# Kernel optimization log

Hardware: AMD Instinct MI355X
Metric: run time of the kernel (lower is better)

The kernel has to match this reference:

```python
import jax, jax.numpy as jnp
import numpy as np

B, L, H = 64, 512, 512  # batch_size, input_size (src len), hidden_size


def setup_inputs() -> dict:
    key = jax.random.key(0)
    ks = jax.random.split(key, 12)
    return {
        "encoder_outputs": jax.random.normal(ks[0], (B, L, H), dtype=jnp.float32),
        "attn_mask": jax.random.randint(ks[1], (B, L), 0, 2, dtype=jnp.int64),
        "hidden": jax.random.normal(ks[2], (B, H), dtype=jnp.float32),
        "coverage": jax.random.uniform(ks[3], (B, L), dtype=jnp.float32),
        # attnLin: Linear(H, H)
        "attn_w": jax.random.normal(ks[4], (H, H), dtype=jnp.float32) * 0.02,
        "attn_b": jax.random.normal(ks[5], (H,), dtype=jnp.float32) * 0.02,
        # decoderAttnLinear: Linear(H, H)
        "dec_w": jax.random.normal(ks[6], (H, H), dtype=jnp.float32) * 0.02,
        "dec_b": jax.random.normal(ks[7], (H,), dtype=jnp.float32) * 0.02,
        # cvgConv: Conv2d(L, L, kernel=(1, H), padding='same') -> weight [L, L, 1, H]
        "cvg_w": jax.random.normal(ks[8], (L, L, 1, H), dtype=jnp.float32) * 0.02,
        "cvg_b": jax.random.normal(ks[9], (L,), dtype=jnp.float32) * 0.02,
        # v parameter (trunc_normal in torch; plain normal is fine as a baseline)
        "v": jax.random.normal(ks[10], (B, H), dtype=jnp.float32),
    }


def reference(encoder_outputs, attn_mask, hidden, coverage,
              attn_w, attn_b, dec_w, dec_b, cvg_w, cvg_b, v):
    # Per-position linear loop in torch == one batched linear over [B, L, H].
    enc_feat = jnp.einsum('blh,oh->blo', encoder_outputs, attn_w) + attn_b  # [B,L,H]
    dec_feat = (hidden @ dec_w.T + dec_b)[:, None, :]                        # [B,1,H]
    # Coverage conv: input is [B, L(channels), 1, 1]; kernel (1, H) with 'same'
    # padding means only kernel column kw = (H-1)//2 ever overlaps the single
    # real (non-zero-padded) pixel, so the conv reduces exactly to a matmul
    # with that weight column plus bias. Same math, no wasted zero-multiplies.
    center = (H - 1) // 2
    w_eff = cvg_w[:, :, 0, center]                                           # [L_out, L_in]
    cov_feat = (coverage @ w_eff.T + cvg_b)[:, :, None]                      # [B,L,1]
    feats = jnp.tanh(enc_feat + dec_feat + cov_feat)                         # [B,L,H]
    scores = jnp.einsum('blh,bh->bl', feats, v)                              # [B,L]
    scores = jnp.where(attn_mask == 1, scores, -jnp.inf)
    attn_weights = jax.nn.softmax(scores, axis=1)                            # [B,L]
    new_coverage = coverage + attn_weights                                   # coverage += aw
    context_vector = jnp.einsum('bl,blh->bh', attn_weights, encoder_outputs) # [B,H]
    return context_vector, attn_weights, new_coverage
```

## Files before the change

### kernel.cpp

```cpp
#include <hip/hip_runtime.h>

#define B_ 64
#define L_ 512
#define H_ 512
#define CENTER 255

typedef float  f32x4  __attribute__((ext_vector_type(4)));
typedef _Float16 f16x8 __attribute__((ext_vector_type(8)));
typedef unsigned short u16x4 __attribute__((ext_vector_type(4)));
typedef unsigned short USH;


__device__ __forceinline__ float fast_tanh(float x) {
    float e = __expf(2.0f * x);
    return 1.0f - 2.0f * __builtin_amdgcn_rcpf(e + 1.0f);
}

__launch_bounds__(512)
__global__ void pre_kernel(const float* __restrict__ cvg_w, const float* __restrict__ cvg_b,
                           const float* __restrict__ coverage,
                           const float* __restrict__ aw, USH* __restrict__ bh16,
                           const float* __restrict__ hidden, const float* __restrict__ dec_w,
                           const float* __restrict__ dec_b,
                           float* __restrict__ dec_feat, float* __restrict__ cov_feat) {
    __shared__ float pool[34304];
    const int bid = blockIdx.x, t = threadIdx.x;
    if (bid < 512) {
        float* wl = pool;
        float* cs = pool + 512;
        const int i = bid;
        wl[t] = cvg_w[((size_t)(i * L_ + t)) * H_ + CENTER];
        #pragma unroll 8
        for (int c = 0; c < 64; ++c)
            cs[t * 65 + c] = coverage[c * L_ + t];
        __syncthreads();
        const int b = t >> 3, jg = t & 7;
        float sum = 0.f;
        #pragma unroll 8
        for (int jj = 0; jj < 64; ++jj) {
            int j = jg * 64 + ((jj + jg * 8) & 63);
            sum += cs[j * 65 + b] * wl[j];
        }
        sum += __shfl_xor(sum, 1, 64);
        sum += __shfl_xor(sum, 2, 64);
        sum += __shfl_xor(sum, 4, 64);
        if (jg == 0) cov_feat[b * L_ + i] = sum + cvg_b[i];
    } else if (bid < 640) {
        int i = (bid - 512) * 512 + t;
        float4 x = *(const float4*)&aw[(size_t)i * 4];
        float xs[4] = {x.x, x.y, x.z, x.w};
        u16x4 h;
        #pragma unroll
        for (int j = 0; j < 4; ++j)
            h[j] = __builtin_bit_cast(USH, (_Float16)xs[j]);
        *(u16x4*)&bh16[(size_t)i * 4] = h;
    } else {
        float* sbuf = pool;
        float* pr   = pool + 512;
        const int blk = bid - 640, b = blk >> 2, qq = blk & 3;
        const int ol = t & 127, part = t >> 7;
        sbuf[t] = hidden[b * H_ + t];
        __syncthreads();
        const float* row  = dec_w + (size_t)(qq * 128 + ol) * H_ + part * 128;
        const float* hseg = sbuf + part * 128;
        float d0 = 0.f, d1 = 0.f, d2 = 0.f, d3 = 0.f;
        #pragma unroll
        for (int k = 0; k < 128; k += 16) {
            float4 w0 = *(const float4*)&row[k];
            float4 w1 = *(const float4*)&row[k + 4];
            float4 w2 = *(const float4*)&row[k + 8];
            float4 w3 = *(const float4*)&row[k + 12];
            d0 += w0.x * hseg[k]      + w0.y * hseg[k + 1]  + w0.z * hseg[k + 2]  + w0.w * hseg[k + 3];
            d1 += w1.x * hseg[k + 4]  + w1.y * hseg[k + 5]  + w1.z * hseg[k + 6]  + w1.w * hseg[k + 7];
            d2 += w2.x * hseg[k + 8]  + w2.y * hseg[k + 9]  + w2.z * hseg[k + 10] + w2.w * hseg[k + 11];
            d3 += w3.x * hseg[k + 12] + w3.y * hseg[k + 13] + w3.z * hseg[k + 14] + w3.w * hseg[k + 15];
        }
        pr[t] = d0 + d1 + d2 + d3;
        __syncthreads();
        if (t < 128)
            dec_feat[b * H_ + qq * 128 + t] = pr[t] + pr[t + 128] + pr[t + 256] + pr[t + 384]
                                              + dec_b[qq * 128 + t];
    }
}

#define BM 128

#define STAGE_B(BUF, KS1)                                                                  \
    {                                                                                      \
        _Pragma("unroll")                                                                  \
        for (int it = 0; it < 2; ++it)                                                     \
            __builtin_amdgcn_global_load_lds(                                              \
                (const __attribute__((address_space(1))) void*)(bh16 + goffB[it] + (KS1) * 32), \
                (__attribute__((address_space(3))) void*)&Bsh[BUF][(wv * 2 + it) * 512],   \
                16, 0, 0);                                                                 \
    }

#define CVTWRITEA(BUF, A4)                                                                 \
    {                                                                                      \
        float axs[4] = {A4.x, A4.y, A4.z, A4.w};                                           \
        u16x4 hh;                                                                          \
        _Pragma("unroll")                                                                  \
        for (int j = 0; j < 4; ++j)                                                        \
            hh[j] = __builtin_bit_cast(USH, (_Float16)axs[j]);                             \
        *(u16x4*)&Ash[BUF][awoff] = hh;                                                    \
    }

__launch_bounds__(1024, 4)
__global__ void fused_score_mfma(const float* __restrict__ enc,
                                 const USH* __restrict__ bh16,
                                 const float* __restrict__ attn_b,
                                 const float* __restrict__ dec_feat,
                                 const float* __restrict__ cov_feat,
                                 const float* __restrict__ v,
                                 float* __restrict__ scores) {
    __shared__ USH Bsh[3][16384];
    __shared__ USH Ash[2][4096];

    const int t  = threadIdx.x;
    const int wv = t >> 6, ln = t & 63;
    const int wr = wv >> 3, wc = wv & 7;
    const int q  = ln >> 4, cl = ln & 15;
    const int m0 = blockIdx.x * BM;
    const int b  = blockIdx.x >> 2;

    int goffB[2];
    #pragma unroll
    for (int it = 0; it < 2; ++it) {
        int c   = wv * 2 + it;
        int srl = ln >> 3;
        int u   = (ln & 7) ^ (srl & 7);
        int n   = c * 16 + srl * 2 + (u >> 2);
        goffB[it] = n * 512 + (u & 3) * 8;
    }
    const int sA   = (((cl & 1) * 4 + q) ^ ((cl >> 1) & 7)) * 8;
    const int aoff = wr * 2048 + (cl >> 1) * 64 + sA;
    const int boff = wc * 2048 + (cl >> 1) * 64 + sA;

    const int arow = t >> 3, akoct = t & 7;
    const int asw  = ((arow & 1) * 4 + (akoct >> 1)) ^ ((arow >> 1) & 7);
    const int awoff = (arow >> 1) * 64 + asw * 8 + (akoct & 1) * 4;
    const float* agsrc = enc + (size_t)(m0 + arow) * H_ + akoct * 4;

    f32x4 acc[4][4];
    #pragma unroll
    for (int mf = 0; mf < 4; ++mf)
        #pragma unroll
        for (int nf = 0; nf < 4; ++nf) acc[mf][nf] = (f32x4){0.f, 0.f, 0.f, 0.f};

    float4 aP = *(const float4*)(agsrc + 32);
    float4 c0 = *(const float4*)agsrc;
    __builtin_amdgcn_sched_barrier(0);
    STAGE_B(0, 0);
    STAGE_B(1, 1);
    __builtin_amdgcn_sched_barrier(0);
    CVTWRITEA(0, c0);
    asm volatile("s_waitcnt lgkmcnt(0)" ::: "memory");
    asm volatile("s_waitcnt vmcnt(2)" ::: "memory");
    __builtin_amdgcn_sched_barrier(0);
    __builtin_amdgcn_s_barrier();

    #pragma unroll
    for (int ks = 0; ks < 16; ++ks) {
        const int curB = ks % 3;
        const int curA = ks & 1, nxtA = curA ^ 1;
        float4 aN;
        if (ks < 14) {
            STAGE_B((ks + 2) % 3, ks + 2);
            aN = *(const float4*)(agsrc + (ks + 2) * 32);
            __builtin_amdgcn_sched_barrier(0);
        }

        f16x8 ah[4];
        #pragma unroll
        for (int mf = 0; mf < 4; ++mf)
            ah[mf] = *(const f16x8*)&Ash[curA][aoff + mf * 512];
        __builtin_amdgcn_s_setprio(1);
        #pragma unroll
        for (int nf = 0; nf < 4; ++nf) {
            f16x8 bh = *(const f16x8*)&Bsh[curB][boff + nf * 512];
            #pragma unroll
            for (int mf = 0; mf < 4; ++mf)
                acc[mf][nf] = __builtin_amdgcn_mfma_f32_16x16x32_f16(ah[mf], bh, acc[mf][nf], 0, 0, 0);
        }
        __builtin_amdgcn_s_setprio(0);

        if (ks < 15) {
            CVTWRITEA(nxtA, aP);
            aP = aN;
            asm volatile("s_waitcnt lgkmcnt(0)" ::: "memory");
            if (ks < 14)
                asm volatile("s_waitcnt vmcnt(3)" ::: "memory");
            else
                asm volatile("s_waitcnt vmcnt(0)" ::: "memory");
            __builtin_amdgcn_sched_barrier(0);
            __builtin_amdgcn_s_barrier();
        }
    }
    __syncthreads();

    float (*scred)[BM] = (float (*)[BM])Ash;
    float addv[4], vvv[4];
    #pragma unroll
    for (int nf = 0; nf < 4; ++nf) {
        int n = wc * 64 + nf * 16 + cl;
        addv[nf] = attn_b[n] + dec_feat[b * H_ + n];
        vvv[nf]  = v[b * H_ + n];
    }
    #pragma unroll
    for (int mf = 0; mf < 4; ++mf) {
        #pragma unroll
        for (int reg = 0; reg < 4; ++reg) {
            int row = wr * 64 + mf * 16 + q * 4 + reg;
            float cf = cov_feat[m0 + row];
            float s = 0.f;
            #pragma unroll
            for (int nf = 0; nf < 4; ++nf)
                s += fast_tanh(acc[mf][nf][reg] + addv[nf] + cf) * vvv[nf];
            s += __shfl_xor(s, 1, 64);
            s += __shfl_xor(s, 2, 64);
            s += __shfl_xor(s, 4, 64);
            s += __shfl_xor(s, 8, 64);
            if (cl == 0) scred[wc][row] = s;
        }
    }
    __syncthreads();
    if (t < BM) {
        float s = 0.f;
        #pragma unroll
        for (int g = 0; g < 8; ++g) s += scred[g][t];
        scores[m0 + t] = s;
    }
}

__launch_bounds__(1024)
__global__ void smctx_kernel(const float* __restrict__ scores, const int* __restrict__ mask,
                             const float* __restrict__ coverage, const float* __restrict__ enc,
                             float* __restrict__ out) {
    __shared__ float w[512];
    __shared__ float red[16];
    __shared__ float red2[16];
    __shared__ float4 cred4[32][32];
    const int bid = blockIdx.x, b = bid >> 2, hc = bid & 3, t = threadIdx.x;
    const int wv = t >> 6, ln = t & 63;

    float sv = 0.f; bool mk = false;
    if (t < 512) {
        mk = (mask[b * L_ + t] == 1);
        sv = scores[b * L_ + t];
    }
    float val = (t < 512 && mk) ? sv : -INFINITY;

    float r = val;
    #pragma unroll
    for (int d = 1; d <= 32; d <<= 1) r = fmaxf(r, __shfl_xor(r, d, 64));
    if (ln == 0) red[wv] = r;
    __syncthreads();
    float gmax = red[0];
    #pragma unroll
    for (int i = 1; i < 16; ++i) gmax = fmaxf(gmax, red[i]);

    float p = (t < 512 && mk) ? __expf(sv - gmax) : 0.f;
    float qq = p;
    #pragma unroll
    for (int d = 1; d <= 32; d <<= 1) qq += __shfl_xor(qq, d, 64);
    if (ln == 0) red2[wv] = qq;
    __syncthreads();
    float tot = 0.f;
    #pragma unroll
    for (int i = 0; i < 16; ++i) tot += red2[i];

    float wt = p / tot;
    if (t < 512) {
        w[t] = wt;
        if (hc == 0) {
            out[B_ * H_ + b * L_ + t] = wt;
            out[B_ * H_ + B_ * L_ + b * L_ + t] = coverage[b * L_ + t] + wt;
        }
    }
    __syncthreads();

    const int c4 = t & 31, rg = t >> 5;
    const float4* ebase = (const float4*)enc
                          + ((size_t)(b * L_ + rg)) * 128 + hc * 32 + c4;
    float4 a4 = {0.f, 0.f, 0.f, 0.f};
    #pragma unroll
    for (int k = 0; k < 16; ++k) {
        float wl_ = w[rg + 32 * k];
        float4 e = ebase[(size_t)(32 * k) * 128];
        a4.x += wl_ * e.x; a4.y += wl_ * e.y; a4.z += wl_ * e.z; a4.w += wl_ * e.w;
    }
    cred4[rg][c4] = a4;
    __syncthreads();
    if (t < 32) {
        float4 s = {0.f, 0.f, 0.f, 0.f};
        #pragma unroll
        for (int g = 0; g < 32; ++g) {
            float4 c = cred4[g][t];
            s.x += c.x; s.y += c.y; s.z += c.z; s.w += c.w;
        }
        *(float4*)&out[b * H_ + hc * 128 + t * 4] = s;
    }
}

extern "C" void kernel_launch(void* const* d_in, const int* in_sizes, int n_in,
                              void* d_out, int out_size, void* d_ws, size_t ws_size,
                              hipStream_t stream) {
    const float* enc      = (const float*)d_in[0];
    const int*   mask     = (const int*)d_in[1];
    const float* hidden   = (const float*)d_in[2];
    const float* coverage = (const float*)d_in[3];
    const float* attn_w   = (const float*)d_in[4];
    const float* attn_b   = (const float*)d_in[5];
    const float* dec_w    = (const float*)d_in[6];
    const float* dec_b    = (const float*)d_in[7];
    const float* cvg_w    = (const float*)d_in[8];
    const float* cvg_b    = (const float*)d_in[9];
    const float* v        = (const float*)d_in[10];
    float* out = (float*)d_out;
    float* ws  = (float*)d_ws;
    float* scores   = ws;
    float* dec_feat = ws + 32768;
    float* cov_feat = ws + 65536;
    USH* bpk = (USH*)(ws + 360448);

    hipLaunchKernelGGL(pre_kernel,       dim3(896),  dim3(512),  0, stream,
                       cvg_w, cvg_b, coverage, attn_w, bpk, hidden, dec_w, dec_b,
                       dec_feat, cov_feat);
    hipLaunchKernelGGL(fused_score_mfma, dim3(256),  dim3(1024), 0, stream,
                       enc, bpk, attn_b, dec_feat, cov_feat, v, scores);
    hipLaunchKernelGGL(smctx_kernel,     dim3(256),  dim3(1024), 0, stream,
                       scores, mask, coverage, enc, out);
}
```

Baseline: 67.71 us.

## Split score GEMM across two N-halves with partial-score reduction in softmax

The fused score kernel now launches a 256x2 grid of 512-thread blocks, each computing half of the hidden (N) dimension and writing partial scores. The softmax/context kernel sums the two partial score arrays. This doubles block count to fill more CUs (256 blocks vs 256 CUs previously with 1024-thread blocks) and halves LDS for B, at the cost of loading and converting the encoder A tile twice, plus an extra partial-score write and read.

```diff
diff --git a/kernel.cpp b/kernel.cpp
--- a/kernel.cpp
+++ b/kernel.cpp
@@ -8,6 +8,7 @@
 typedef float  f32x4  __attribute__((ext_vector_type(4)));
 typedef _Float16 f16x8 __attribute__((ext_vector_type(8)));
 typedef unsigned short u16x4 __attribute__((ext_vector_type(4)));
+typedef unsigned short u16x8 __attribute__((ext_vector_type(8)));
 typedef unsigned short USH;
 
 
@@ -95,33 +96,35 @@
                 16, 0, 0);                                                                 \
     }
 
-#define CVTWRITEA(BUF, A4)                                                                 \
+#define CVTWRITEA2(BUF, A4a, A4b)                                                          \
     {                                                                                      \
-        float axs[4] = {A4.x, A4.y, A4.z, A4.w};                                           \
-        u16x4 hh;                                                                          \
+        float axs[8] = {A4a.x, A4a.y, A4a.z, A4a.w, A4b.x, A4b.y, A4b.z, A4b.w};           \
+        u16x8 hh;                                                                          \
         _Pragma("unroll")                                                                  \
-        for (int j = 0; j < 4; ++j)                                                        \
+        for (int j = 0; j < 8; ++j)                                                        \
             hh[j] = __builtin_bit_cast(USH, (_Float16)axs[j]);                             \
-        *(u16x4*)&Ash[BUF][awoff] = hh;                                                    \
-    }
-
-__launch_bounds__(1024, 4)
+        *(u16x8*)&Ash[BUF][awoff] = hh;                                                    \
+    }
+
+__launch_bounds__(512, 4)
 __global__ void fused_score_mfma(const float* __restrict__ enc,
                                  const USH* __restrict__ bh16,
                                  const float* __restrict__ attn_b,
                                  const float* __restrict__ dec_feat,
                                  const float* __restrict__ cov_feat,
                                  const float* __restrict__ v,
-                                 float* __restrict__ scores) {
-    __shared__ USH Bsh[3][16384];
+                                 float* __restrict__ spart) {
+    __shared__ USH Bsh[3][8192];
     __shared__ USH Ash[2][4096];
 
     const int t  = threadIdx.x;
     const int wv = t >> 6, ln = t & 63;
-    const int wr = wv >> 3, wc = wv & 7;
+    const int wr = wv >> 2, wc = wv & 3;
     const int q  = ln >> 4, cl = ln & 15;
-    const int m0 = blockIdx.x * BM;
-    const int b  = blockIdx.x >> 2;
+    const int mt = blockIdx.x, half = blockIdx.y;
+    const int m0 = mt * BM;
+    const int b  = mt >> 2;
+    const int n0 = half * 256;
 
     int goffB[2];
     #pragma unroll
@@ -129,17 +132,17 @@
         int c   = wv * 2 + it;
         int srl = ln >> 3;
         int u   = (ln & 7) ^ (srl & 7);
-        int n   = c * 16 + srl * 2 + (u >> 2);
+        int n   = n0 + c * 16 + srl * 2 + (u >> 2);
         goffB[it] = n * 512 + (u & 3) * 8;
     }
     const int sA   = (((cl & 1) * 4 + q) ^ ((cl >> 1) & 7)) * 8;
     const int aoff = wr * 2048 + (cl >> 1) * 64 + sA;
     const int boff = wc * 2048 + (cl >> 1) * 64 + sA;
 
-    const int arow = t >> 3, akoct = t & 7;
-    const int asw  = ((arow & 1) * 4 + (akoct >> 1)) ^ ((arow >> 1) & 7);
-    const int awoff = (arow >> 1) * 64 + asw * 8 + (akoct & 1) * 4;
-    const float* agsrc = enc + (size_t)(m0 + arow) * H_ + akoct * 4;
+    const int arow = t >> 2, ak4 = t & 3;
+    const int asw  = ((arow & 1) * 4 + ak4) ^ ((arow >> 1) & 7);
+    const int awoff = (arow >> 1) * 64 + asw * 8;
+    const float* agsrc = enc + (size_t)(m0 + arow) * H_ + ak4 * 8;
 
     f32x4 acc[4][4];
     #pragma unroll
@@ -147,13 +150,15 @@
         #pragma unroll
         for (int nf = 0; nf < 4; ++nf) acc[mf][nf] = (f32x4){0.f, 0.f, 0.f, 0.f};
 
-    float4 aP = *(const float4*)(agsrc + 32);
-    float4 c0 = *(const float4*)agsrc;
+    float4 aPa = *(const float4*)(agsrc + 32);
+    float4 aPb = *(const float4*)(agsrc + 36);
+    float4 c0a = *(const float4*)agsrc;
+    float4 c0b = *(const float4*)(agsrc + 4);
     __builtin_amdgcn_sched_barrier(0);
     STAGE_B(0, 0);
     STAGE_B(1, 1);
     __builtin_amdgcn_sched_barrier(0);
-    CVTWRITEA(0, c0);
+    CVTWRITEA2(0, c0a, c0b);
     asm volatile("s_waitcnt lgkmcnt(0)" ::: "memory");
     asm volatile("s_waitcnt vmcnt(2)" ::: "memory");
     __builtin_amdgcn_sched_barrier(0);
@@ -163,10 +168,11 @@
     for (int ks = 0; ks < 16; ++ks) {
         const int curB = ks % 3;
         const int curA = ks & 1, nxtA = curA ^ 1;
-        float4 aN;
+        float4 aNa, aNb;
         if (ks < 14) {
             STAGE_B((ks + 2) % 3, ks + 2);
-            aN = *(const float4*)(agsrc + (ks + 2) * 32);
+            aNa = *(const float4*)(agsrc + (ks + 2) * 32);
+            aNb = *(const float4*)(agsrc + (ks + 2) * 32 + 4);
             __builtin_amdgcn_sched_barrier(0);
         }
 
@@ -185,11 +191,11 @@
         __builtin_amdgcn_s_setprio(0);
 
         if (ks < 15) {
-            CVTWRITEA(nxtA, aP);
-            aP = aN;
+            CVTWRITEA2(nxtA, aPa, aPb);
+            aPa = aNa; aPb = aNb;
             asm volatile("s_waitcnt lgkmcnt(0)" ::: "memory");
             if (ks < 14)
-                asm volatile("s_waitcnt vmcnt(3)" ::: "memory");
+                asm volatile("s_waitcnt vmcnt(4)" ::: "memory");
             else
                 asm volatile("s_waitcnt vmcnt(0)" ::: "memory");
             __builtin_amdgcn_sched_barrier(0);
@@ -202,7 +208,7 @@
     float addv[4], vvv[4];
     #pragma unroll
     for (int nf = 0; nf < 4; ++nf) {
-        int n = wc * 64 + nf * 16 + cl;
+        int n = n0 + wc * 64 + nf * 16 + cl;
         addv[nf] = attn_b[n] + dec_feat[b * H_ + n];
         vvv[nf]  = v[b * H_ + n];
     }
@@ -227,13 +233,13 @@
     if (t < BM) {
         float s = 0.f;
         #pragma unroll
-        for (int g = 0; g < 8; ++g) s += scred[g][t];
-        scores[m0 + t] = s;
+        for (int g = 0; g < 4; ++g) s += scred[g][t];
+        spart[half * (B_ * L_) + m0 + t] = s;
     }
 }
 
 __launch_bounds__(1024)
-__global__ void smctx_kernel(const float* __restrict__ scores, const int* __restrict__ mask,
+__global__ void smctx_kernel(const float* __restrict__ spart, const int* __restrict__ mask,
                              const float* __restrict__ coverage, const float* __restrict__ enc,
                              float* __restrict__ out) {
     __shared__ float w[512];
@@ -246,7 +252,7 @@
     float sv = 0.f; bool mk = false;
     if (t < 512) {
         mk = (mask[b * L_ + t] == 1);
-        sv = scores[b * L_ + t];
+        sv = spart[b * L_ + t] + spart[B_ * L_ + b * L_ + t];
     }
     float val = (t < 512 && mk) ? sv : -INFINITY;
 
@@ -318,16 +324,16 @@
     const float* v        = (const float*)d_in[10];
     float* out = (float*)d_out;
     float* ws  = (float*)d_ws;
-    float* scores   = ws;
     float* dec_feat = ws + 32768;
     float* cov_feat = ws + 65536;
+    float* spart    = ws + 98304;
     USH* bpk = (USH*)(ws + 360448);
 
-    hipLaunchKernelGGL(pre_kernel,       dim3(896),  dim3(512),  0, stream,
+    hipLaunchKernelGGL(pre_kernel,       dim3(896),     dim3(512),  0, stream,
                        cvg_w, cvg_b, coverage, attn_w, bpk, hidden, dec_w, dec_b,
                        dec_feat, cov_feat);
-    hipLaunchKernelGGL(fused_score_mfma, dim3(256),  dim3(1024), 0, stream,
-                       enc, bpk, attn_b, dec_feat, cov_feat, v, scores);
-    hipLaunchKernelGGL(smctx_kernel,     dim3(256),  dim3(1024), 0, stream,
-                       scores, mask, coverage, enc, out);
-}
+    hipLaunchKernelGGL(fused_score_mfma, dim3(256, 2),  dim3(512),  0, stream,
+                       enc, bpk, attn_b, dec_feat, cov_feat, v, spart);
+    hipLaunchKernelGGL(smctx_kernel,     dim3(256),     dim3(1024), 0, stream,
+                       spart, mask, coverage, enc, out);
+}
```

Measured after the change: 67.43 us. About the same (-0.4%).
